# Kernel tuning notes

Hardware: AMD Instinct MI355X
Metric: run time of the kernel (lower is better)

The kernel has to match this reference:

```python
import jax, jax.numpy as jnp
import numpy as np

NUM_GENES = 9229
NUM_FEATURES = 3
BATCH = 4096


def setup_inputs() -> dict:
    key = jax.random.key(0)
    k1, k2, k3 = jax.random.split(key, 3)
    x = jax.random.normal(k1, (BATCH, NUM_GENES * NUM_FEATURES), dtype=jnp.float32)
    weights = jax.random.normal(k2, (NUM_GENES * NUM_FEATURES,), dtype=jnp.float32)
    bias = 0.1 * jax.random.normal(k3, (NUM_GENES,), dtype=jnp.float32)
    return {"x": x, "weights": weights, "bias": bias}


def reference(x, weights, bias):
    # Block-diagonal scatter + mm is equivalent to a per-gene weighted sum
    # over the feature dimension:
    # x: [B, G*F] -> [B, G, F]; weights: [G*F] -> [G, F]
    B = x.shape[0]
    xg = x.reshape(B, NUM_GENES, NUM_FEATURES)
    wg = weights.reshape(NUM_GENES, NUM_FEATURES)
    out = jnp.einsum("bgf,gf->bg", xg, wg) + bias  # [B, G]
    return out
```

## Files before the change

### kernel.cpp

```cpp
#include <hip/hip_runtime.h>


#define NUM_GENES 9229
#define TOTAL_OUT (4096 * 9229)

__global__ __launch_bounds__(256) void diag_layer_kernel(
    const float* __restrict__ x,
    const float* __restrict__ w,
    const float* __restrict__ bias,
    float* __restrict__ out) {

    const unsigned n_items = TOTAL_OUT / 4;
    unsigned item = blockIdx.x * blockDim.x + threadIdx.x;
    const unsigned stride = gridDim.x * blockDim.x;

    for (; item < n_items; item += stride) {
        const unsigned obase = item * 4u;
        const unsigned xbase = obase * 3u;

        const float4 v0 = *reinterpret_cast<const float4*>(x + xbase);
        const float4 v1 = *reinterpret_cast<const float4*>(x + xbase + 4);
        const float4 v2 = *reinterpret_cast<const float4*>(x + xbase + 8);

        const float xe[12] = {v0.x, v0.y, v0.z, v0.w,
                              v1.x, v1.y, v1.z, v1.w,
                              v2.x, v2.y, v2.z, v2.w};

        float r[4];
#pragma unroll
        for (int k = 0; k < 4; ++k) {
            const unsigned i = obase + (unsigned)k;
            const unsigned g = i % NUM_GENES;
            const float* wg = w + 3u * g;
            r[k] = fmaf(xe[3 * k], wg[0],
                   fmaf(xe[3 * k + 1], wg[1],
                   fmaf(xe[3 * k + 2], wg[2], bias[g])));
        }

        *reinterpret_cast<float4*>(out + obase) =
            make_float4(r[0], r[1], r[2], r[3]);
    }
}

extern "C" void kernel_launch(void* const* d_in, const int* in_sizes, int n_in,
                              void* d_out, int out_size, void* d_ws, size_t ws_size,
                              hipStream_t stream) {
    const float* x    = (const float*)d_in[0];
    const float* w    = (const float*)d_in[1];
    const float* bias = (const float*)d_in[2];
    float* out        = (float*)d_out;

    const int block = 256;
    const int grid  = 2048;

    diag_layer_kernel<<<grid, block, 0, stream>>>(x, w, bias, out);
}
```

Measured before the change: 135.2 us.

## Tile over gene chunks with register-resident weights and LDS-staged input rows

Restructures the kernel so each block owns a tile of 923 genes and a group of 20 batch rows. Weights and bias for the tile are loaded once into registers, and each row's input slice is staged into LDS with float4 loads before the per-gene dot products are computed. This removes the per-element modulo and the repeated weight and bias gathers. In exchange it adds two barriers per row, scalar (non-vectorized) output stores, and fewer, longer-running blocks.

```diff
diff --git a/kernel.cpp b/kernel.cpp
--- a/kernel.cpp
+++ b/kernel.cpp
@@ -1,44 +1,77 @@
 #include <hip/hip_runtime.h>
 
 
-#define NUM_GENES 9229
-#define TOTAL_OUT (4096 * 9229)
+#define G       9229
+#define GF      (9229 * 3)
+#define B       4096
+#define GT      923
+#define NT      10
+#define BLK     256
+#define RPB     20
+#define RGROUPS 205
+#define STAGE_F4 694
 
-__global__ __launch_bounds__(256) void diag_layer_kernel(
+__global__ __launch_bounds__(BLK) void diag_layer_kernel(
     const float* __restrict__ x,
     const float* __restrict__ w,
     const float* __restrict__ bias,
     float* __restrict__ out) {
 
-    const unsigned n_items = TOTAL_OUT / 4;
-    unsigned item = blockIdx.x * blockDim.x + threadIdx.x;
-    const unsigned stride = gridDim.x * blockDim.x;
+    __shared__ float lds[STAGE_F4 * 4];
 
-    for (; item < n_items; item += stride) {
-        const unsigned obase = item * 4u;
-        const unsigned xbase = obase * 3u;
+    const int t    = threadIdx.x;
+    const int tile = (int)blockIdx.x % NT;
+    const int rg   = (int)blockIdx.x / NT;
+    const int g0   = tile * GT;
+    const int gtloc = min(GT, G - g0);
 
-        const float4 v0 = *reinterpret_cast<const float4*>(x + xbase);
-        const float4 v1 = *reinterpret_cast<const float4*>(x + xbase + 4);
-        const float4 v2 = *reinterpret_cast<const float4*>(x + xbase + 8);
+    float wreg[4][3];
+    float breg[4];
+#pragma unroll
+    for (int j = 0; j < 4; ++j) {
+        const int gl = t + BLK * j;
+        const int gc = g0 + ((gl < gtloc) ? gl : 0);
+        wreg[j][0] = w[3 * gc];
+        wreg[j][1] = w[3 * gc + 1];
+        wreg[j][2] = w[3 * gc + 2];
+        breg[j]    = bias[gc];
+    }
 
-        const float xe[12] = {v0.x, v0.y, v0.z, v0.w,
-                              v1.x, v1.y, v1.z, v1.w,
-                              v2.x, v2.y, v2.z, v2.w};
+    const unsigned x_f4_max = (unsigned)B * (unsigned)GF / 4u - 1u;
 
-        float r[4];
+    const int row_begin = rg * RPB;
+    const int row_end   = min(row_begin + RPB, B);
+
+    for (int b = row_begin; b < row_end; ++b) {
+        const unsigned row_off  = (unsigned)b * (unsigned)GF + (unsigned)(3 * g0);
+        const unsigned abase_f4 = row_off >> 2;
+        const unsigned shift    = row_off & 3u;
+
+        __syncthreads();
 #pragma unroll
-        for (int k = 0; k < 4; ++k) {
-            const unsigned i = obase + (unsigned)k;
-            const unsigned g = i % NUM_GENES;
-            const float* wg = w + 3u * g;
-            r[k] = fmaf(xe[3 * k], wg[0],
-                   fmaf(xe[3 * k + 1], wg[1],
-                   fmaf(xe[3 * k + 2], wg[2], bias[g])));
+        for (int j = 0; j < 3; ++j) {
+            const int idx = t + BLK * j;
+            if (idx < STAGE_F4) {
+                unsigned gi = abase_f4 + (unsigned)idx;
+                gi = (gi > x_f4_max) ? x_f4_max : gi;
+                reinterpret_cast<float4*>(lds)[idx] =
+                    reinterpret_cast<const float4*>(x)[gi];
+            }
         }
+        __syncthreads();
 
-        *reinterpret_cast<float4*>(out + obase) =
-            make_float4(r[0], r[1], r[2], r[3]);
+        const unsigned ob = (unsigned)b * (unsigned)G + (unsigned)g0;
+#pragma unroll
+        for (int j = 0; j < 4; ++j) {
+            const int gl = t + BLK * j;
+            if (gl < gtloc) {
+                const float* xp = lds + shift + 3 * gl;
+                const float r = fmaf(xp[0], wreg[j][0],
+                                fmaf(xp[1], wreg[j][1],
+                                fmaf(xp[2], wreg[j][2], breg[j])));
+                out[ob + (unsigned)gl] = r;
+            }
+        }
     }
 }
 
@@ -50,8 +83,5 @@
     const float* bias = (const float*)d_in[2];
     float* out        = (float*)d_out;
 
-    const int block = 256;
-    const int grid  = 2048;
-
-    diag_layer_kernel<<<grid, block, 0, stream>>>(x, w, bias, out);
+    diag_layer_kernel<<<NT * RGROUPS, BLK, 0, stream>>>(x, w, bias, out);
 }
```

Measured after the change: 148.8 us. 10.0% more time.

## Tile the diagonal layer over gene groups and row chunks, reusing weights in registers

Applied to the files above, without the earlier changes.

The flat grid-stride loop is replaced by a 2D decomposition. Each thread owns four consecutive genes and walks 16 batch rows. Weights and bias for those genes are loaded once into registers, which removes the per-element modulo and the repeated weight/bias gathers. The cost is float4 loads and stores at row offsets that are not 16-byte aligned (the row lengths are odd), plus a scalar tail path for the last gene. It also adds a fixed grid with some idle threads in the last gene group.

```diff
diff --git a/kernel.cpp b/kernel.cpp
--- a/kernel.cpp
+++ b/kernel.cpp
@@ -1,44 +1,60 @@
 #include <hip/hip_runtime.h>
 
 
-#define NUM_GENES 9229
-#define TOTAL_OUT (4096 * 9229)
+#define G    9229
+#define GF   27687
+#define B    4096
+#define GB   2308
+#define BLK  256
+#define GBG  10
+#define RPC  16
+#define NRC  (B / RPC)
 
-__global__ __launch_bounds__(256) void diag_layer_kernel(
+__global__ __launch_bounds__(BLK) void diag_layer_kernel(
     const float* __restrict__ x,
     const float* __restrict__ w,
     const float* __restrict__ bias,
     float* __restrict__ out) {
 
-    const unsigned n_items = TOTAL_OUT / 4;
-    unsigned item = blockIdx.x * blockDim.x + threadIdx.x;
-    const unsigned stride = gridDim.x * blockDim.x;
+    const int t   = threadIdx.x;
+    const int gbg = (int)blockIdx.x % GBG;
+    const int rc  = (int)blockIdx.x / GBG;
+    const int gb  = gbg * BLK + t;
+    if (gb >= GB) return;
 
-    for (; item < n_items; item += stride) {
-        const unsigned obase = item * 4u;
-        const unsigned xbase = obase * 3u;
+    const int row0 = rc * RPC;
 
-        const float4 v0 = *reinterpret_cast<const float4*>(x + xbase);
-        const float4 v1 = *reinterpret_cast<const float4*>(x + xbase + 4);
-        const float4 v2 = *reinterpret_cast<const float4*>(x + xbase + 8);
+    if (gb < GB - 1) {
+        const float4 w0 = *reinterpret_cast<const float4*>(w + 12 * gb);
+        const float4 w1 = *reinterpret_cast<const float4*>(w + 12 * gb + 4);
+        const float4 w2 = *reinterpret_cast<const float4*>(w + 12 * gb + 8);
+        const float4 bv = *reinterpret_cast<const float4*>(bias + 4 * gb);
 
-        const float xe[12] = {v0.x, v0.y, v0.z, v0.w,
-                              v1.x, v1.y, v1.z, v1.w,
-                              v2.x, v2.y, v2.z, v2.w};
-
-        float r[4];
-#pragma unroll
-        for (int k = 0; k < 4; ++k) {
-            const unsigned i = obase + (unsigned)k;
-            const unsigned g = i % NUM_GENES;
-            const float* wg = w + 3u * g;
-            r[k] = fmaf(xe[3 * k], wg[0],
-                   fmaf(xe[3 * k + 1], wg[1],
-                   fmaf(xe[3 * k + 2], wg[2], bias[g])));
+#pragma unroll 4
+        for (int r = 0; r < RPC; ++r) {
+            const unsigned b  = (unsigned)(row0 + r);
+            const unsigned xb = b * (unsigned)GF + 12u * (unsigned)gb;
+            const float4 v0 = *reinterpret_cast<const float4*>(x + xb);
+            const float4 v1 = *reinterpret_cast<const float4*>(x + xb + 4);
+            const float4 v2 = *reinterpret_cast<const float4*>(x + xb + 8);
+            float4 o;
+            o.x = fmaf(v0.x, w0.x, fmaf(v0.y, w0.y, fmaf(v0.z, w0.z, bv.x)));
+            o.y = fmaf(v0.w, w0.w, fmaf(v1.x, w1.x, fmaf(v1.y, w1.y, bv.y)));
+            o.z = fmaf(v1.z, w1.z, fmaf(v1.w, w1.w, fmaf(v2.x, w2.x, bv.z)));
+            o.w = fmaf(v2.y, w2.y, fmaf(v2.z, w2.z, fmaf(v2.w, w2.w, bv.w)));
+            *reinterpret_cast<float4*>(out + (size_t)b * G + 4u * (unsigned)gb) = o;
         }
-
-        *reinterpret_cast<float4*>(out + obase) =
-            make_float4(r[0], r[1], r[2], r[3]);
+    } else {
+        const float wa = w[3 * (G - 1)];
+        const float wb_ = w[3 * (G - 1) + 1];
+        const float wc = w[3 * (G - 1) + 2];
+        const float bz = bias[G - 1];
+        for (int r = 0; r < RPC; ++r) {
+            const unsigned b  = (unsigned)(row0 + r);
+            const unsigned xb = b * (unsigned)GF + 3u * (G - 1);
+            out[(size_t)b * G + (G - 1)] =
+                fmaf(x[xb], wa, fmaf(x[xb + 1], wb_, fmaf(x[xb + 2], wc, bz)));
+        }
     }
 }
 
@@ -50,8 +66,5 @@
     const float* bias = (const float*)d_in[2];
     float* out        = (float*)d_out;
 
-    const int block = 256;
-    const int grid  = 2048;
-
-    diag_layer_kernel<<<grid, block, 0, stream>>>(x, w, bias, out);
+    diag_layer_kernel<<<GBG * NRC, BLK, 0, stream>>>(x, w, bias, out);
 }
```

Result: slower. 146.8 us (+8.6%).

## Assign wavefronts to fixed gene windows with register-resident weights and shuffles

Applied to the files above, without the earlier changes.

Each wavefront now owns a 256-gene window and a strided set of batch rows. It loads that window's weights and bias into registers once, then reuses them for every row it handles. The per-gene triple sums that cross float4 boundaries are formed with cross-lane shuffles, so the per-element modulo and weight/bias gathers go away. The 13 leftover genes are handled by a scalar path. Row bases are odd multiples of floats, so the float4 loads and stores become unaligned, which may cost extra memory transactions on a kernel that is already bandwidth-bound.

```diff
diff --git a/kernel.cpp b/kernel.cpp
--- a/kernel.cpp
+++ b/kernel.cpp
@@ -1,8 +1,12 @@
 #include <hip/hip_runtime.h>
 
 
-#define NUM_GENES 9229
-#define TOTAL_OUT (4096 * 9229)
+#define G     9229
+#define GF    27687
+#define NB    4096
+#define NWIN  36
+#define SLOTS 221
+#define NW    (37 * SLOTS)
 
 __global__ __launch_bounds__(256) void diag_layer_kernel(
     const float* __restrict__ x,
@@ -10,35 +14,79 @@
     const float* __restrict__ bias,
     float* __restrict__ out) {
 
-    const unsigned n_items = TOTAL_OUT / 4;
-    unsigned item = blockIdx.x * blockDim.x + threadIdx.x;
-    const unsigned stride = gridDim.x * blockDim.x;
+    const int t = (int)(threadIdx.x & 63);
+    const int W = (int)blockIdx.x * 4 + (int)(threadIdx.x >> 6);
+    if (W >= NW) return;
+    const int win = W % 37;
+    const int s   = W / 37;
 
-    for (; item < n_items; item += stride) {
-        const unsigned obase = item * 4u;
-        const unsigned xbase = obase * 3u;
+    if (win < NWIN) {
+        const int F0 = 768 * win;
+        const float4 w0 = *reinterpret_cast<const float4*>(w + F0 + 4 * t);
+        const float4 w1 = *reinterpret_cast<const float4*>(w + F0 + 256 + 4 * t);
+        const float4 w2 = *reinterpret_cast<const float4*>(w + F0 + 512 + 4 * t);
+        const float4 bv = *reinterpret_cast<const float4*>(bias + 256 * win + 4 * t);
 
-        const float4 v0 = *reinterpret_cast<const float4*>(x + xbase);
-        const float4 v1 = *reinterpret_cast<const float4*>(x + xbase + 4);
-        const float4 v2 = *reinterpret_cast<const float4*>(x + xbase + 8);
+        const int tm   = t % 3;
+        const bool last = (t == 63);
+        const int srcA = (3 * t) & 63;
+        const int srcC = (3 * t + 1) & 63;
+        const int srcD = (3 * t + 2) & 63;
 
-        const float xe[12] = {v0.x, v0.y, v0.z, v0.w,
-                              v1.x, v1.y, v1.z, v1.w,
-                              v2.x, v2.y, v2.z, v2.w};
+#pragma unroll 2
+        for (int r = s; r < NB; r += SLOTS) {
+            const float* xr = x + r * GF + F0;
+            const float4 v0 = *reinterpret_cast<const float4*>(xr + 4 * t);
+            const float4 v1 = *reinterpret_cast<const float4*>(xr + 256 + 4 * t);
+            const float4 v2 = *reinterpret_cast<const float4*>(xr + 512 + 4 * t);
 
-        float r[4];
-#pragma unroll
-        for (int k = 0; k < 4; ++k) {
-            const unsigned i = obase + (unsigned)k;
-            const unsigned g = i % NUM_GENES;
-            const float* wg = w + 3u * g;
-            r[k] = fmaf(xe[3 * k], wg[0],
-                   fmaf(xe[3 * k + 1], wg[1],
-                   fmaf(xe[3 * k + 2], wg[2], bias[g])));
+            const float a0 = v0.x * w0.x, a1 = v0.y * w0.y, a2 = v0.z * w0.z, a3 = v0.w * w0.w;
+            const float q01_0 = a0 + a1, q23_0 = a2 + a3;
+            const float q012_0 = q01_0 + a2, q123_0 = q23_0 + a1;
+            const float b0 = v1.x * w1.x, b1 = v1.y * w1.y, b2 = v1.z * w1.z, b3 = v1.w * w1.w;
+            const float q01_1 = b0 + b1, q23_1 = b2 + b3;
+            const float q012_1 = q01_1 + b2, q123_1 = q23_1 + b1;
+            const float c0 = v2.x * w2.x, c1 = v2.y * w2.y, c2 = v2.z * w2.z, c3 = v2.w * w2.w;
+            const float q01_2 = c0 + c1, q23_2 = c2 + c3;
+            const float q012_2 = q01_2 + c2, q123_2 = q23_2 + c1;
+
+            const float s0 = (tm == 1) ? q01_0 : a0;
+            const float s1 = (tm == 0) ? q01_1 : b0;
+            const float s2 = (tm == 2) ? q01_2 : c0;
+            const float r0 = __shfl(s0, (t + 1) & 63);
+            const float r1 = __shfl(s1, (t + 1) & 63);
+            const float r2 = __shfl(s2, (t + 1) & 63);
+            const float E0 = last ? r1 : r0;
+            const float E1 = last ? r2 : r1;
+            const float E2 = r2;
+
+            const float bb0 = a3 + E0, bb1 = b3 + E1, bb2 = c3 + E2;
+            const float cc0 = q23_0 + E0, cc1 = q23_1 + E1, cc2 = q23_2 + E2;
+
+            const float A = (tm == 0) ? q012_0 : (tm == 2) ? q012_1 : q012_2;
+            const float Bv = (tm == 0) ? bb0   : (tm == 2) ? bb1   : bb2;
+            const float C = (tm == 1) ? cc0   : (tm == 0) ? cc1   : cc2;
+            const float D = (tm == 2) ? q123_0 : (tm == 1) ? q123_1 : q123_2;
+
+            float4 o;
+            o.x = __shfl(A,  srcA) + bv.x;
+            o.y = __shfl(Bv, srcA) + bv.y;
+            o.z = __shfl(C,  srcC) + bv.z;
+            o.w = __shfl(D,  srcD) + bv.w;
+
+            *reinterpret_cast<float4*>(out + r * G + 256 * win + 4 * t) = o;
         }
-
-        *reinterpret_cast<float4*>(out + obase) =
-            make_float4(r[0], r[1], r[2], r[3]);
+    } else {
+        if (t < 13) {
+            const int g = 9216 + t;
+            const float wa = w[3 * g], wb = w[3 * g + 1], wc = w[3 * g + 2];
+            const float bz = bias[g];
+            for (int r = s; r < NB; r += SLOTS) {
+                const float* xr = x + r * GF + 3 * g;
+                out[r * G + g] =
+                    fmaf(xr[0], wa, fmaf(xr[1], wb, fmaf(xr[2], wc, bz)));
+            }
+        }
     }
 }
 
@@ -50,8 +98,5 @@
     const float* bias = (const float*)d_in[2];
     float* out        = (float*)d_out;
 
-    const int block = 256;
-    const int grid  = 2048;
-
-    diag_layer_kernel<<<grid, block, 0, stream>>>(x, w, bias, out);
+    diag_layer_kernel<<<2048, 256, 0, stream>>>(x, w, bias, out);
 }
```

New measurement: 125.9 us. 6.9% less time.
